# Kernel tuning notes

Measured on AMD Instinct MI355X. Metric: run time of the kernel, lower is better.

The kernel has to match this reference:

```python
import jax, jax.numpy as jnp
import numpy as np

B, S, H, E, V, EXTRA = 128, 512, 1024, 1024, 50000, 500
EPS = 1e-8


def setup_inputs() -> dict:
    key = jax.random.key(0)
    ks = jax.random.split(key, 32)
    sc = 0.02
    n = lambda k, sh: (jax.random.normal(k, sh, jnp.float32) * sc)
    return {
        'inputs': jax.random.randint(ks[0], (B, 1), 0, V),
        'dec_hidden': n(ks[1], (1, B, H)),
        'enc_outputs': n(ks[2], (B, S, H)),
        'enc_padding_mask': jnp.zeros((B, S), jnp.float32),
        'context_vector_t1': n(ks[3], (B, H)),
        'enc_batch_extend_vocab': jax.random.randint(ks[4], (B, S), 0, V + EXTRA),
        'extra_zeros': jnp.zeros((B, EXTRA), jnp.float32),
        'coverage': jax.random.uniform(ks[5], (B, S), jnp.float32) * 0.1,
        # parameters
        'embed': n(ks[6], (V, E)),
        'ln_g': jnp.ones((E,), jnp.float32),
        'ln_b': jnp.zeros((E,), jnp.float32),
        'xc_W': n(ks[7], (E, H + E)), 'xc_b': jnp.zeros((E,), jnp.float32),
        'W_ih': n(ks[8], (3 * H, E)), 'W_hh': n(ks[9], (3 * H, H)),
        'b_ih': jnp.zeros((3 * H,), jnp.float32), 'b_hh': jnp.zeros((3 * H,), jnp.float32),
        'Wh': n(ks[10], (H, H)),
        'Ws': n(ks[11], (H, H)), 'Ws_b': jnp.zeros((H,), jnp.float32),
        'Wc': n(ks[12], (H, 1)),
        'Vv': n(ks[13], (H,)),
        'pg_W': n(ks[14], (2 * H + E,)), 'pg_b': jnp.zeros((1,), jnp.float32),
        'out1_W': n(ks[15], (H, 2 * H)), 'out1_b': jnp.zeros((H,), jnp.float32),
        'out2_W': n(ks[16], (V, H)), 'out2_b': jnp.zeros((V,), jnp.float32),
    }


def _layernorm(x, g, b):
    mu = jnp.mean(x, axis=-1, keepdims=True)
    var = jnp.mean(jnp.square(x - mu), axis=-1, keepdims=True)
    return (x - mu) / jnp.sqrt(var + 1e-5) * g + b


def reference(inputs, dec_hidden, enc_outputs, enc_padding_mask, context_vector_t1,
              enc_batch_extend_vocab, extra_zeros, coverage,
              embed, ln_g, ln_b, xc_W, xc_b, W_ih, W_hh, b_ih, b_hh,
              Wh, Ws, Ws_b, Wc, Vv, pg_W, pg_b, out1_W, out1_b, out2_W, out2_b):
    # embedding + layernorm: [B, E]
    x = _layernorm(embed[inputs[:, 0]], ln_g, ln_b)
    # x_context: Linear(H+E -> E)
    x = jnp.concatenate([x, context_vector_t1], axis=1) @ xc_W.T + xc_b

    # single GRU step (torch gate order r, z, n)
    h0 = dec_hidden[0]  # [B, H]
    gx = x @ W_ih.T + b_ih
    gh = h0 @ W_hh.T + b_hh
    r = jax.nn.sigmoid(gx[:, :H] + gh[:, :H])
    z = jax.nn.sigmoid(gx[:, H:2 * H] + gh[:, H:2 * H])
    nn_ = jnp.tanh(gx[:, 2 * H:] + r * gh[:, 2 * H:])
    s_t = (1.0 - z) * nn_ + z * h0  # [B, H]; dec_output == s_t for 1-layer GRU
    dec_output = s_t

    # Bahdanau additive attention with coverage
    enc_feat = jnp.einsum('bsh,kh->bsk', enc_outputs, Wh)           # [B,S,H]
    dec_feat = s_t @ Ws.T + Ws_b                                     # [B,H]
    cov_feat = coverage[:, :, None] * Wc[:, 0][None, None, :]        # [B,S,H]
    e_t = jnp.einsum('bsh,h->bs', jnp.tanh(enc_feat + dec_feat[:, None, :] + cov_feat), Vv)
    atten_dist = jax.nn.softmax(e_t + enc_padding_mask, axis=1)      # [B,S]
    h_t = jnp.einsum('bs,bsh->bh', atten_dist, enc_outputs)          # [B,H]
    coverage_next = coverage + atten_dist

    # pointer generator gate
    p_gen_in = jnp.concatenate([h_t, s_t, x], axis=1)                # [B, 2H+E]
    p_gen = jnp.clip(jax.nn.sigmoid(p_gen_in @ pg_W + pg_b), EPS, None)[:, None]  # [B,1]

    # vocab distribution
    s_t_h_t = jnp.concatenate([dec_output, h_t], axis=1)             # [B,2H]
    logits = (s_t_h_t @ out1_W.T + out1_b) @ out2_W.T + out2_b       # [B,V]
    vocab_dist = jax.nn.softmax(logits, axis=1)

    # mix + scatter-add copy distribution over extended vocab
    vocab_dist_ = jnp.concatenate([p_gen * vocab_dist, extra_zeros], axis=1)  # [B, V+EXTRA]
    atten_dist_ = (1.0 - p_gen) * atten_dist
    rows = jnp.arange(B)[:, None]
    final_dist = vocab_dist_.at[rows, enc_batch_extend_vocab].add(atten_dist_)
    final_dist = jnp.clip(final_dist, EPS, None)

    coverage_loss = jnp.sum(jnp.minimum(atten_dist, coverage_next), axis=1)  # [B]
    return (jnp.log(final_dist), s_t[None], h_t, coverage_next, coverage_loss)
```

## Files before the change

### kernel.cpp

```cpp
#include <hip/hip_runtime.h>
#include <hip/hip_bf16.h>
#include <stdint.h>

#define B_ 128
#define S_ 512
#define H_ 1024
#define E_ 1024
#define V_ 50000
#define EXTRA_ 500
#define VE_ 50500
#define EPS_ 1e-8f

typedef __attribute__((ext_vector_type(4))) float f32x4;
typedef __attribute__((ext_vector_type(8))) short bf16x8;

__device__ __forceinline__ unsigned short f2bf(float f) {
    unsigned u = __builtin_bit_cast(unsigned, f);
    u = (u + 0x7FFFu + ((u >> 16) & 1u)) >> 16;
    return (unsigned short)u;
}

__device__ __forceinline__ bf16x8 pack8(const float* f) {
    union { bf16x8 v; unsigned short s[8]; } u;
#pragma unroll
    for (int i = 0; i < 8; ++i) u.s[i] = f2bf(f[i]);
    return u.v;
}

__device__ __forceinline__ float bf2f(unsigned short s) {
    unsigned u = (unsigned)s << 16;
    return __builtin_bit_cast(float, u);
}

__device__ __forceinline__ float fast_tanh(float x) {
    x = fminf(fmaxf(x, -15.f), 15.f);
    float e = __expf(2.f * x);
    return __fdividef(e - 1.f, e + 1.f);
}

__device__ __forceinline__ void gload16(const void* g, void* l) {
    __builtin_amdgcn_global_load_lds(
        reinterpret_cast<const __attribute__((address_space(1))) unsigned int*>(
            reinterpret_cast<uintptr_t>(g)),
        reinterpret_cast<__attribute__((address_space(3))) unsigned int*>(
            reinterpret_cast<uintptr_t>(l)),
        16, 0, 0);
}

__global__ __launch_bounds__(256) void cvt_bf16_kernel(const float* __restrict__ in,
                                                       unsigned short* __restrict__ out) {
    int i = (blockIdx.x * 256 + threadIdx.x) * 8;
    float f[8];
    *(float4*)f     = *(const float4*)(in + i);
    *(float4*)(f+4) = *(const float4*)(in + i + 4);
    union { uint4 v; unsigned short s[8]; } u;
#pragma unroll
    for (int j = 0; j < 8; ++j) u.s[j] = f2bf(f[j]);
    *(uint4*)(out + i) = u.v;
}

__global__ __launch_bounds__(256) void embed_ln_kernel(
    const int* __restrict__ tok, const float* __restrict__ embed,
    const float* __restrict__ g, const float* __restrict__ beta,
    const float* __restrict__ ctx, float* __restrict__ x_cat)
{
    __shared__ float red[256];
    int b = blockIdx.x, t = threadIdx.x;
    const float* row = embed + (size_t)tok[b] * E_;
    float v[4];
    float s = 0.f;
#pragma unroll
    for (int i = 0; i < 4; ++i) { v[i] = row[t + i*256]; s += v[i]; }
    red[t] = s; __syncthreads();
    for (int o = 128; o > 0; o >>= 1) { if (t < o) red[t] += red[t+o]; __syncthreads(); }
    float mu = red[0] * (1.f/E_);
    __syncthreads();
    s = 0.f;
#pragma unroll
    for (int i = 0; i < 4; ++i) { float d = v[i]-mu; s += d*d; }
    red[t] = s; __syncthreads();
    for (int o = 128; o > 0; o >>= 1) { if (t < o) red[t] += red[t+o]; __syncthreads(); }
    float inv = rsqrtf(red[0]*(1.f/E_) + 1e-5f);
    float* xrow = x_cat + (size_t)b * 2048;
#pragma unroll
    for (int i = 0; i < 4; ++i) {
        int j = t + i*256;
        xrow[j] = (v[i]-mu)*inv*g[j] + beta[j];
        xrow[1024 + j] = ctx[b*1024 + j];
    }
}

__global__ __launch_bounds__(256) void gemm128_kernel(
    const float* __restrict__ A, const float* __restrict__ W,
    const float* __restrict__ bias, float* __restrict__ C, float* __restrict__ C1,
    int N, int K, int ldc, int kchunk)
{
    __shared__ char Ab[128*64*2];
    __shared__ char Wb[64*64*2];
    const int t = threadIdx.x;
    const int wid = t >> 6, lane = t & 63;
    const int waveM = wid >> 1, waveN = wid & 1;
    const int lq = lane >> 4, lr = lane & 15;
    const int n0 = blockIdx.x * 64;
    const int kbeg = blockIdx.y * kchunk, kend = kbeg + kchunk;
    f32x4 acc[4][2];
#pragma unroll
    for (int i = 0; i < 4; ++i)
#pragma unroll
        for (int j = 0; j < 2; ++j) acc[i][j] = (f32x4){0.f,0.f,0.f,0.f};
    for (int kc = kbeg; kc < kend; kc += 64) {
        __syncthreads();
#pragma unroll
        for (int i = 0; i < 4; ++i) {
            int c = t + i*256;
            int row = c >> 3, k8 = (c & 7) << 3;
            const float* src = A + (size_t)row*K + kc + k8;
            float f[8];
            *(float4*)f     = *(const float4*)src;
            *(float4*)(f+4) = *(const float4*)(src+4);
            int byte = row*128 + ((k8*2) ^ ((row&7)<<4));
            *(bf16x8*)(Ab + byte) = pack8(f);
        }
#pragma unroll
        for (int i = 0; i < 2; ++i) {
            int c = t + i*256;
            int row = c >> 3, k8 = (c & 7) << 3;
            int n = n0 + row;
            float f[8] = {0,0,0,0,0,0,0,0};
            if (n < N) {
                const float* src = W + (size_t)n*K + kc + k8;
                *(float4*)f     = *(const float4*)src;
                *(float4*)(f+4) = *(const float4*)(src+4);
            }
            int byte = row*128 + ((k8*2) ^ ((row&7)<<4));
            *(bf16x8*)(Wb + byte) = pack8(f);
        }
        __syncthreads();
#pragma unroll
        for (int kf = 0; kf < 2; ++kf) {
            int kk2 = (kf*32 + (lq<<3)) * 2;
            bf16x8 bfr[2];
#pragma unroll
            for (int nf = 0; nf < 2; ++nf) {
                int r = waveN*32 + nf*16 + lr;
                bfr[nf] = *(const bf16x8*)(Wb + r*128 + (kk2 ^ ((r&7)<<4)));
            }
#pragma unroll
            for (int mf = 0; mf < 4; ++mf) {
                int r = waveM*64 + mf*16 + lr;
                bf16x8 afr = *(const bf16x8*)(Ab + r*128 + (kk2 ^ ((r&7)<<4)));
#pragma unroll
                for (int nf = 0; nf < 2; ++nf)
                    acc[mf][nf] = __builtin_amdgcn_mfma_f32_16x16x32_bf16(afr, bfr[nf], acc[mf][nf], 0, 0, 0);
            }
        }
    }
    float* Cp = (blockIdx.y == 0) ? C : (C1 + (size_t)(blockIdx.y - 1) * 128 * (size_t)ldc);
    bool addb = (bias != nullptr) && (blockIdx.y == 0);
#pragma unroll
    for (int mf = 0; mf < 4; ++mf)
#pragma unroll
        for (int nf = 0; nf < 2; ++nf) {
            int n = n0 + waveN*32 + nf*16 + lr;
            if (n < N) {
                float bv = addb ? bias[n] : 0.f;
#pragma unroll
                for (int r = 0; r < 4; ++r) {
                    int m = waveM*64 + mf*16 + (lq<<2) + r;
                    Cp[(size_t)m*ldc + n] = acc[mf][nf][r] + bv;
                }
            }
        }
}

__global__ __launch_bounds__(256) void reduce4_kernel(
    const float* __restrict__ in, float* __restrict__ out, int len)
{
    int i = blockIdx.x*256 + threadIdx.x;
    if (i < len) out[i] = in[i] + in[len+i] + in[2*len+i] + in[3*len+i];
}

__global__ __launch_bounds__(256) void gru_gate_kernel(
    const float* __restrict__ gxp, const float* __restrict__ ghp,
    const float* __restrict__ h0, float* __restrict__ s_t)
{
    int i = blockIdx.x*256 + threadIdx.x;
    int b = i >> 10, h = i & 1023;
    const float* gx0 = gxp + (size_t)b*3072;
    const float* gx1 = gx0 + 393216;
    const float* gh0 = ghp + (size_t)b*3072;
    const float* gh1 = gh0 + 393216;
    float grx = gx0[h] + gx1[h],        grh = gh0[h] + gh1[h];
    float gzx = gx0[h+1024]+gx1[h+1024], gzh = gh0[h+1024]+gh1[h+1024];
    float gnx = gx0[h+2048]+gx1[h+2048], gnh = gh0[h+2048]+gh1[h+2048];
    float r = 1.f/(1.f+__expf(-(grx + grh)));
    float z = 1.f/(1.f+__expf(-(gzx + gzh)));
    float n = fast_tanh(gnx + r*gnh);
    s_t[i] = (1.f-z)*n + z*h0[i];
}

__global__ __launch_bounds__(256,4) void attn_gemm_bf16_kernel(
    const unsigned short* __restrict__ encb,
    const unsigned short* __restrict__ whb,
    const float* __restrict__ dec_feat, const float* __restrict__ coverage,
    const float* __restrict__ Wc, const float* __restrict__ Vv,
    float* __restrict__ e_part)
{
    __shared__ char Ab[128*128];
    __shared__ char Bb[128*128];
    const int t = threadIdx.x;
    const int wid = t >> 6, lane = t & 63;
    const int waveM = wid >> 1, waveN = wid & 1;
    const int lq = lane >> 4, lr = lane & 15;
    int bid = blockIdx.x;
    int wg = (bid & 7) * 512 + (bid >> 3);
    const int nt = wg & 7, mt = wg >> 3;
    const int m0 = mt * 128, n0 = nt * 128;
    const int b = m0 >> 9;

    const int grow = wid*8 + (lane >> 3);
    const int gk16 = (lane & 7) ^ ((lane >> 3) & 7);
    const unsigned short* asrc = encb + (size_t)(m0 + grow)*H_ + gk16*8;
    const unsigned short* bsrc = whb  + (size_t)(n0 + grow)*H_ + gk16*8;
    char* aldst = Ab + wid*1024;
    char* bldst = Bb + wid*1024;

    f32x4 acc[4][4];
#pragma unroll
    for (int i = 0; i < 4; ++i)
#pragma unroll
        for (int j = 0; j < 4; ++j) acc[i][j] = (f32x4){0.f,0.f,0.f,0.f};

    for (int kc = 0; kc < 1024; kc += 64) {
        __syncthreads();
#pragma unroll
        for (int i = 0; i < 4; ++i) {
            gload16(asrc + kc + i*32*H_, aldst + i*4096);
            gload16(bsrc + kc + i*32*H_, bldst + i*4096);
        }
        __syncthreads();
#pragma unroll
        for (int kf = 0; kf < 2; ++kf) {
            const int koff = kf*64 + lq*16;
            bf16x8 bfr[4];
#pragma unroll
            for (int nf = 0; nf < 4; ++nf) {
                int r = waveN*64 + nf*16 + lr;
                bfr[nf] = *(const bf16x8*)(Bb + r*128 + (koff ^ ((r&7)<<4)));
            }
#pragma unroll
            for (int mf = 0; mf < 4; ++mf) {
                int r = waveM*64 + mf*16 + lr;
                bf16x8 afr = *(const bf16x8*)(Ab + r*128 + (koff ^ ((r&7)<<4)));
#pragma unroll
                for (int nf = 0; nf < 4; ++nf)
                    acc[mf][nf] = __builtin_amdgcn_mfma_f32_16x16x32_bf16(afr, bfr[nf], acc[mf][nf], 0, 0, 0);
            }
        }
    }
    float cv[4][4];
#pragma unroll
    for (int mf = 0; mf < 4; ++mf)
#pragma unroll
        for (int r = 0; r < 4; ++r) {
            int m = m0 + waveM*64 + mf*16 + lq*4 + r;
            cv[mf][r] = coverage[b*S_ + (m & 511)];
        }
    float e_acc[4][4] = {};
#pragma unroll
    for (int nf = 0; nf < 4; ++nf) {
        int n = n0 + waveN*64 + nf*16 + lr;
        float df = dec_feat[b*H_ + n];
        float wc = Wc[n];
        float vv = Vv[n];
#pragma unroll
        for (int mf = 0; mf < 4; ++mf)
#pragma unroll
            for (int r = 0; r < 4; ++r)
                e_acc[mf][r] += fast_tanh(acc[mf][nf][r] + df + cv[mf][r]*wc) * vv;
    }
#pragma unroll
    for (int msk = 1; msk < 16; msk <<= 1)
#pragma unroll
        for (int mf = 0; mf < 4; ++mf)
#pragma unroll
            for (int r = 0; r < 4; ++r)
                e_acc[mf][r] += __shfl_xor(e_acc[mf][r], msk);
    __syncthreads();
    float* el = (float*)Ab;
    if (lr == 0) {
#pragma unroll
        for (int mf = 0; mf < 4; ++mf)
#pragma unroll
            for (int r = 0; r < 4; ++r)
                el[waveN*128 + waveM*64 + mf*16 + lq*4 + r] = e_acc[mf][r];
    }
    __syncthreads();
    if (t < 128)
        e_part[(size_t)nt*65536 + m0 + t] = el[t] + el[128 + t];
}

__global__ __launch_bounds__(512,4) void attn_gemm_f32_kernel(
    const float* __restrict__ enc, const float* __restrict__ Wh,
    const float* __restrict__ dec_feat, const float* __restrict__ coverage,
    const float* __restrict__ Wc, const float* __restrict__ Vv,
    float* __restrict__ e_part)
{
    __shared__ char Ab[128*64*2];
    __shared__ char Bb[256*64*2];
    __shared__ float e_lds[4][128];
    const int t = threadIdx.x;
    const int wid = t >> 6, lane = t & 63;
    const int waveM = wid >> 2, waveN = wid & 3;
    const int lq = lane >> 4, lr = lane & 15;
    int bid = blockIdx.x;
    int wg = (bid & 7) * 256 + (bid >> 3);
    const int mt = wg >> 2, nt = wg & 3;
    const int m0 = mt * 128, n0 = nt * 256;
    const int b = m0 >> 9;
    const int arow = t >> 2, ak0 = (t & 3) * 16;
    const int brow = t >> 1, bk0 = (t & 1) * 32;
    f32x4 acc[4][4];
#pragma unroll
    for (int i = 0; i < 4; ++i)
#pragma unroll
        for (int j = 0; j < 4; ++j) acc[i][j] = (f32x4){0.f,0.f,0.f,0.f};
    for (int kc = 0; kc < 1024; kc += 64) {
        __syncthreads();
        {
            const float* src = enc + (size_t)(m0 + arow)*H_ + kc + ak0;
            float f[16];
            *(float4*)(f)    = *(const float4*)(src);
            *(float4*)(f+4)  = *(const float4*)(src+4);
            *(float4*)(f+8)  = *(const float4*)(src+8);
            *(float4*)(f+12) = *(const float4*)(src+12);
            char* dst = Ab + arow*128;
            int sw = (arow & 7) << 4;
            *(bf16x8*)(dst + ((ak0*2)      ^ sw)) = pack8(f);
            *(bf16x8*)(dst + ((ak0*2 + 16) ^ sw)) = pack8(f+8);
        }
        {
            const float* src = Wh + (size_t)(n0 + brow)*H_ + kc + bk0;
            char* dst = Bb + brow*128;
            int sw = (brow & 7) << 4;
            float f[16];
            *(float4*)(f)    = *(const float4*)(src);
            *(float4*)(f+4)  = *(const float4*)(src+4);
            *(float4*)(f+8)  = *(const float4*)(src+8);
            *(float4*)(f+12) = *(const float4*)(src+12);
            *(bf16x8*)(dst + ((bk0*2)      ^ sw)) = pack8(f);
            *(bf16x8*)(dst + ((bk0*2 + 16) ^ sw)) = pack8(f+8);
            *(float4*)(f)    = *(const float4*)(src+16);
            *(float4*)(f+4)  = *(const float4*)(src+20);
            *(float4*)(f+8)  = *(const float4*)(src+24);
            *(float4*)(f+12) = *(const float4*)(src+28);
            *(bf16x8*)(dst + ((bk0*2 + 32) ^ sw)) = pack8(f);
            *(bf16x8*)(dst + ((bk0*2 + 48) ^ sw)) = pack8(f+8);
        }
        __syncthreads();
#pragma unroll
        for (int kf = 0; kf < 2; ++kf) {
            const int koff = kf*64 + lq*16;
            bf16x8 bfr[4];
#pragma unroll
            for (int nf = 0; nf < 4; ++nf) {
                int r = waveN*64 + nf*16 + lr;
                bfr[nf] = *(const bf16x8*)(Bb + r*128 + (koff ^ ((r&7)<<4)));
            }
#pragma unroll
            for (int mf = 0; mf < 4; ++mf) {
                int r = waveM*64 + mf*16 + lr;
                bf16x8 afr = *(const bf16x8*)(Ab + r*128 + (koff ^ ((r&7)<<4)));
#pragma unroll
                for (int nf = 0; nf < 4; ++nf)
                    acc[mf][nf] = __builtin_amdgcn_mfma_f32_16x16x32_bf16(afr, bfr[nf], acc[mf][nf], 0, 0, 0);
            }
        }
    }
    float cv[4][4];
#pragma unroll
    for (int mf = 0; mf < 4; ++mf)
#pragma unroll
        for (int r = 0; r < 4; ++r) {
            int m = m0 + waveM*64 + mf*16 + lq*4 + r;
            cv[mf][r] = coverage[b*S_ + (m & 511)];
        }
    float e_acc[4][4] = {};
#pragma unroll
    for (int nf = 0; nf < 4; ++nf) {
        int n = n0 + waveN*64 + nf*16 + lr;
        float df = dec_feat[b*H_ + n];
        float wc = Wc[n];
        float vv = Vv[n];
#pragma unroll
        for (int mf = 0; mf < 4; ++mf)
#pragma unroll
            for (int r = 0; r < 4; ++r)
                e_acc[mf][r] += fast_tanh(acc[mf][nf][r] + df + cv[mf][r]*wc) * vv;
    }
#pragma unroll
    for (int msk = 1; msk < 16; msk <<= 1)
#pragma unroll
        for (int mf = 0; mf < 4; ++mf)
#pragma unroll
            for (int r = 0; r < 4; ++r)
                e_acc[mf][r] += __shfl_xor(e_acc[mf][r], msk);
    if (lr == 0) {
#pragma unroll
        for (int mf = 0; mf < 4; ++mf)
#pragma unroll
            for (int r = 0; r < 4; ++r)
                e_lds[waveN][waveM*64 + mf*16 + lq*4 + r] = e_acc[mf][r];
    }
    __syncthreads();
    if (t < 128)
        e_part[(size_t)nt*65536 + m0 + t] = e_lds[0][t] + e_lds[1][t] + e_lds[2][t] + e_lds[3][t];
}

__global__ __launch_bounds__(256) void attn_softmax_kernel(
    const float* __restrict__ e_part, int np, const float* __restrict__ mask,
    const float* __restrict__ cov, float* __restrict__ att,
    float* __restrict__ cov_next, float* __restrict__ loss)
{
    __shared__ float red[256];
    int b = blockIdx.x, t = threadIdx.x;
    int i1 = b*S_ + t, i2 = i1 + 256;
    float e1 = mask[i1], e2 = mask[i2];
    for (int p = 0; p < np; ++p) { e1 += e_part[(size_t)p*65536 + i1]; e2 += e_part[(size_t)p*65536 + i2]; }
    red[t] = fmaxf(e1, e2); __syncthreads();
    for (int o = 128; o > 0; o >>= 1) { if (t < o) red[t] = fmaxf(red[t], red[t+o]); __syncthreads(); }
    float m = red[0]; __syncthreads();
    float a1 = __expf(e1-m), a2 = __expf(e2-m);
    red[t] = a1+a2; __syncthreads();
    for (int o = 128; o > 0; o >>= 1) { if (t < o) red[t] += red[t+o]; __syncthreads(); }
    float inv = 1.f/red[0]; __syncthreads();
    a1 *= inv; a2 *= inv;
    att[i1] = a1; att[i2] = a2;
    float c1 = cov[i1]+a1, c2 = cov[i2]+a2;
    cov_next[i1] = c1; cov_next[i2] = c2;
    red[t] = fminf(a1,c1)+fminf(a2,c2); __syncthreads();
    for (int o = 128; o > 0; o >>= 1) { if (t < o) red[t] += red[t+o]; __syncthreads(); }
    if (t == 0) loss[b] = red[0];
}

__global__ __launch_bounds__(256) void context_part_bf16_kernel(
    const float* __restrict__ att, const unsigned short* __restrict__ encb, float* __restrict__ hq)
{
    __shared__ float asl[128];
    int b = blockIdx.x, sub = blockIdx.y;
    int hh = sub & 1, q = sub >> 1;
    int t = threadIdx.x;
    if (t < 128) asl[t] = att[b*S_ + q*128 + t];
    __syncthreads();
    int h = hh*512 + t*2;
    const unsigned short* ep = encb + (size_t)b*S_*H_ + (size_t)q*128*H_ + h;
    float a0 = 0.f, a1 = 0.f;
#pragma unroll 4
    for (int s = 0; s < 128; ++s) {
        union { unsigned u; unsigned short s2[2]; } v;
        v.u = *(const unsigned*)(ep + (size_t)s*H_);
        float w = asl[s];
        a0 += w*bf2f(v.s2[0]); a1 += w*bf2f(v.s2[1]);
    }
    float* o = hq + ((size_t)q*B_ + b)*H_ + h;
    o[0] = a0; o[1] = a1;
}

__global__ __launch_bounds__(256) void context_part_f32_kernel(
    const float* __restrict__ att, const float* __restrict__ enc, float* __restrict__ hq)
{
    __shared__ float asl[128];
    int b = blockIdx.x, sub = blockIdx.y;
    int hh = sub & 1, q = sub >> 1;
    int t = threadIdx.x;
    if (t < 128) asl[t] = att[b*S_ + q*128 + t];
    __syncthreads();
    int h = hh*512 + t*2;
    const float* ep = enc + (size_t)b*S_*H_ + (size_t)q*128*H_ + h;
    float a0 = 0.f, a1 = 0.f;
#pragma unroll 4
    for (int s = 0; s < 128; ++s) {
        float2 v = *(const float2*)(ep + (size_t)s*H_);
        float w = asl[s];
        a0 += w*v.x; a1 += w*v.y;
    }
    float* o = hq + ((size_t)q*B_ + b)*H_ + h;
    o[0] = a0; o[1] = a1;
}

__global__ __launch_bounds__(256) void pgen_kernel(
    const float* __restrict__ h_t, const float* __restrict__ s_t, const float* __restrict__ x,
    const float* __restrict__ pgW, const float* __restrict__ pgb,
    float* __restrict__ pgen, float* __restrict__ A2)
{
    __shared__ float red[256];
    int b = blockIdx.x, t = threadIdx.x;
    float s = 0.f;
#pragma unroll
    for (int i = 0; i < 12; ++i) {
        int j = t + i*256;
        float v = (j < 1024) ? h_t[b*1024+j] : (j < 2048 ? s_t[b*1024 + j-1024] : x[b*1024 + j-2048]);
        s += v * pgW[j];
    }
    red[t] = s; __syncthreads();
    for (int o = 128; o > 0; o >>= 1) { if (t < o) red[t] += red[t+o]; __syncthreads(); }
    if (t == 0) {
        float p = 1.f/(1.f+__expf(-(red[0] + pgb[0])));
        pgen[b] = fmaxf(p, EPS_);
    }
#pragma unroll
    for (int i = 0; i < 8; ++i) {
        int j = t + i*256;
        A2[(size_t)b*2048 + j] = (j < 1024) ? s_t[b*1024+j] : h_t[b*1024+j-1024];
    }
}

__global__ __launch_bounds__(256) void vocab_pass1_kernel(
    const float* __restrict__ logits, float2* __restrict__ mpart)
{
    __shared__ float rm[256], rl[256];
    int b = blockIdx.x, c = blockIdx.y, t = threadIdx.x;
    int lo = c * 12625;
    int hi = min(lo + 12625, V_);
    const float* row = logits + (size_t)b*VE_;
    float m = -1e30f, l = 0.f;
    for (int i = lo + t; i < hi; i += 256) {
        float v = row[i];
        if (v > m) { l = l*__expf(m-v) + 1.f; m = v; }
        else l += __expf(v-m);
    }
    rm[t] = m; rl[t] = l; __syncthreads();
    for (int o = 128; o > 0; o >>= 1) {
        if (t < o) {
            float m1 = rm[t], m2 = rm[t+o];
            float M = fmaxf(m1, m2);
            rl[t] = rl[t]*__expf(m1-M) + rl[t+o]*__expf(m2-M);
            rm[t] = M;
        }
        __syncthreads();
    }
    if (t == 0) mpart[b*4 + c] = make_float2(rm[0], rl[0]);
}

__global__ __launch_bounds__(256) void vocab_pass2_kernel(
    const float* __restrict__ logits, const float2* __restrict__ mpart,
    const float* __restrict__ pgen, const int* __restrict__ ebev,
    const float* __restrict__ att, float* __restrict__ out0)
{
    __shared__ unsigned bmap[395];
    __shared__ unsigned hkey[1024];
    __shared__ float hval[1024];
    int b = blockIdx.x, c = blockIdx.y, t = threadIdx.x;
    int lo = c * 12625, hi = lo + 12625;
    float2 p0 = mpart[b*4+0], p1 = mpart[b*4+1], p2 = mpart[b*4+2], p3 = mpart[b*4+3];
    float M = fmaxf(fmaxf(p0.x, p1.x), fmaxf(p2.x, p3.x));
    float L = p0.y*__expf(p0.x-M) + p1.y*__expf(p1.x-M) + p2.y*__expf(p2.x-M) + p3.y*__expf(p3.x-M);
    float pg = pgen[b];
    float inv = pg / L;
    for (int i = t; i < 395; i += 256) bmap[i] = 0u;
    for (int i = t; i < 1024; i += 256) { hkey[i] = 0xFFFFFFFFu; hval[i] = 0.f; }
    __syncthreads();
    for (int s = t; s < 512; s += 256) {
        int col = ebev[b*S_ + s];
        if (col >= lo && col < hi) {
            float v = (1.f - pg) * att[b*S_ + s];
            unsigned cl = (unsigned)(col - lo);
            atomicOr(&bmap[cl >> 5], 1u << (cl & 31));
            unsigned slot = (cl * 2654435761u >> 16) & 1023u;
            while (true) {
                unsigned old = atomicCAS(&hkey[slot], 0xFFFFFFFFu, cl);
                if (old == 0xFFFFFFFFu || old == cl) { atomicAdd(&hval[slot], v); break; }
                slot = (slot + 1) & 1023u;
            }
        }
    }
    __syncthreads();
    const float* row = logits + (size_t)b*VE_;
    float* orow = out0 + (size_t)b*VE_;
    for (int i = lo + t; i < hi; i += 256) {
        float base = 0.f;
        if (i < V_) base = __expf(row[i] - M) * inv;
        unsigned cl = (unsigned)(i - lo);
        if (bmap[cl >> 5] & (1u << (cl & 31))) {
            unsigned slot = (cl * 2654435761u >> 16) & 1023u;
            while (hkey[slot] != cl) slot = (slot + 1) & 1023u;
            base += hval[slot];
        }
        orow[i] = __logf(fmaxf(base, EPS_));
    }
}

extern "C" void kernel_launch(void* const* d_in, const int* in_sizes, int n_in,
                              void* d_out, int out_size, void* d_ws, size_t ws_size,
                              hipStream_t stream) {
    const int*   tok        = (const int*)d_in[0];
    const float* dec_hidden = (const float*)d_in[1];
    const float* enc        = (const float*)d_in[2];
    const float* mask       = (const float*)d_in[3];
    const float* ctx1       = (const float*)d_in[4];
    const int*   ebev       = (const int*)d_in[5];
    const float* cov        = (const float*)d_in[7];
    const float* embed      = (const float*)d_in[8];
    const float* ln_g       = (const float*)d_in[9];
    const float* ln_b       = (const float*)d_in[10];
    const float* xc_W       = (const float*)d_in[11];
    const float* xc_b       = (const float*)d_in[12];
    const float* W_ih       = (const float*)d_in[13];
    const float* W_hh       = (const float*)d_in[14];
    const float* b_ih       = (const float*)d_in[15];
    const float* b_hh       = (const float*)d_in[16];
    const float* Wh         = (const float*)d_in[17];
    const float* Ws         = (const float*)d_in[18];
    const float* Ws_b       = (const float*)d_in[19];
    const float* Wc         = (const float*)d_in[20];
    const float* Vv         = (const float*)d_in[21];
    const float* pg_W       = (const float*)d_in[22];
    const float* pg_b       = (const float*)d_in[23];
    const float* out1_W     = (const float*)d_in[24];
    const float* out1_b     = (const float*)d_in[25];
    const float* out2_W     = (const float*)d_in[26];
    const float* out2_b     = (const float*)d_in[27];

    float* out      = (float*)d_out;
    float* s_t      = out + 6464000;
    float* h_t      = out + 6595072;
    float* cov_next = out + 6726144;
    float* loss     = out + 6791680;

    const size_t ENC_SLOTS = 33554432, WH_SLOTS = 524288;
    const size_t BASE_SLOTS = 5178496;
    const size_t need = (ENC_SLOTS + WH_SLOTS + BASE_SLOTS) * 4;
    const bool bf16_path = (ws_size >= need);

    float* wsf = (float*)d_ws;
    unsigned short* enc_bf = (unsigned short*)d_ws;
    unsigned short* wh_bf  = (unsigned short*)(wsf + ENC_SLOTS);
    float* base     = bf16_path ? (wsf + ENC_SLOTS + WH_SLOTS) : wsf;
    float* x_cat    = base;
    float* x_part   = base + 262144;
    float* x        = base + 786432;
    float* gx_part  = base + 917504;
    float* gh_part  = base + 1703936;
    float* ds_part  = base + 2490368;
    float* dec_feat = base + 3014656;
    float* e_part   = base + 3145728;
    float* att      = base + 3670016;
    float* pgen     = base + 3735552;
    float* A2       = base + 3735680;
    float* h2_part  = base + 3997824;
    float* h2       = base + 4522112;
    float* hq       = base + 4653184;
    float2* mpart   = (float2*)(base + 5177472);

    if (bf16_path) {
        cvt_bf16_kernel<<<32768, 256, 0, stream>>>(enc, enc_bf);
        cvt_bf16_kernel<<<512, 256, 0, stream>>>(Wh, wh_bf);
    }
    embed_ln_kernel<<<128, 256, 0, stream>>>(tok, embed, ln_g, ln_b, ctx1, x_cat);
    gemm128_kernel<<<dim3(16,4), 256, 0, stream>>>(x_cat, xc_W, xc_b, x_part, x_part + 131072, 1024, 2048, 1024, 512);
    reduce4_kernel<<<512, 256, 0, stream>>>(x_part, x, 131072);
    gemm128_kernel<<<dim3(48,2), 256, 0, stream>>>(x, W_ih, b_ih, gx_part, gx_part + 393216, 3072, 1024, 3072, 512);
    gemm128_kernel<<<dim3(48,2), 256, 0, stream>>>(dec_hidden, W_hh, b_hh, gh_part, gh_part + 393216, 3072, 1024, 3072, 512);
    gru_gate_kernel<<<512, 256, 0, stream>>>(gx_part, gh_part, dec_hidden, s_t);
    gemm128_kernel<<<dim3(16,4), 256, 0, stream>>>(s_t, Ws, Ws_b, ds_part, ds_part + 131072, 1024, 1024, 1024, 256);
    reduce4_kernel<<<512, 256, 0, stream>>>(ds_part, dec_feat, 131072);

    int npart;
    if (bf16_path) {
        attn_gemm_bf16_kernel<<<4096, 256, 0, stream>>>(enc_bf, wh_bf, dec_feat, cov, Wc, Vv, e_part);
        npart = 8;
    } else {
        attn_gemm_f32_kernel<<<2048, 512, 0, stream>>>(enc, Wh, dec_feat, cov, Wc, Vv, e_part);
        npart = 4;
    }
    attn_softmax_kernel<<<128, 256, 0, stream>>>(e_part, npart, mask, cov, att, cov_next, loss);
    dim3 g8(128, 8);
    if (bf16_path)
        context_part_bf16_kernel<<<g8, 256, 0, stream>>>(att, enc_bf, hq);
    else
        context_part_f32_kernel<<<g8, 256, 0, stream>>>(att, enc, hq);
    reduce4_kernel<<<512, 256, 0, stream>>>(hq, h_t, 131072);
    pgen_kernel<<<128, 256, 0, stream>>>(h_t, s_t, x, pg_W, pg_b, pgen, A2);
    gemm128_kernel<<<dim3(16,4), 256, 0, stream>>>(A2, out1_W, out1_b, h2_part, h2_part + 131072, 1024, 2048, 1024, 512);
    reduce4_kernel<<<512, 256, 0, stream>>>(h2_part, h2, 131072);

    gemm128_kernel<<<dim3(782,1), 256, 0, stream>>>(h2, out2_W, out2_b, out, nullptr, 50000, 1024, VE_, 1024);
    vocab_pass1_kernel<<<dim3(128,4), 256, 0, stream>>>(out, mpart);
    vocab_pass2_kernel<<<dim3(128,4), 256, 0, stream>>>(out, mpart, pgen, ebev, att, out);
}
```

Measured before the change: 532.1 us.

## Fuse split-K partial reductions into consumers and widen bf16 context loads

The split-K reduction for dec_feat is folded into the attention GEMM epilogue, and the h_t reduction is folded into pgen_kernel, which also builds A2 in the same pass. This removes two reduce4 launches and their intermediate buffers. The bf16 context kernel now loads 16-byte vectors with 4 blocks per batch row, combining two half-sequence partials in LDS. The attention GEMM launch bound rises to 5 waves per SIMD, which may force register spills.

```diff
diff --git a/kernel.cpp b/kernel.cpp
--- a/kernel.cpp
+++ b/kernel.cpp
@@ -92,7 +92,7 @@
 
 __global__ __launch_bounds__(256) void gemm128_kernel(
     const float* __restrict__ A, const float* __restrict__ W,
-    const float* __restrict__ bias, float* __restrict__ C, float* __restrict__ C1,
+    const float* __restrict__ bias, float* __restrict__ C,
     int N, int K, int ldc, int kchunk)
 {
     __shared__ char Ab[128*64*2];
@@ -155,7 +155,7 @@
             }
         }
     }
-    float* Cp = (blockIdx.y == 0) ? C : (C1 + (size_t)(blockIdx.y - 1) * 128 * (size_t)ldc);
+    float* Cp = C + (size_t)blockIdx.y * 128 * (size_t)ldc;
     bool addb = (bias != nullptr) && (blockIdx.y == 0);
 #pragma unroll
     for (int mf = 0; mf < 4; ++mf)
@@ -199,10 +199,11 @@
     s_t[i] = (1.f-z)*n + z*h0[i];
 }
 
-__global__ __launch_bounds__(256,4) void attn_gemm_bf16_kernel(
+__global__ __launch_bounds__(256,5) void attn_gemm_bf16_kernel(
     const unsigned short* __restrict__ encb,
     const unsigned short* __restrict__ whb,
-    const float* __restrict__ dec_feat, const float* __restrict__ coverage,
+    const float* __restrict__ ds_part,
+    const float* __restrict__ coverage,
     const float* __restrict__ Wc, const float* __restrict__ Vv,
     float* __restrict__ e_part)
 {
@@ -270,7 +271,8 @@
 #pragma unroll
     for (int nf = 0; nf < 4; ++nf) {
         int n = n0 + waveN*64 + nf*16 + lr;
-        float df = dec_feat[b*H_ + n];
+        const float* dsp = ds_part + b*H_ + n;
+        float df = dsp[0] + dsp[131072] + dsp[262144] + dsp[393216];
         float wc = Wc[n];
         float vv = Vv[n];
 #pragma unroll
@@ -302,7 +304,7 @@
 
 __global__ __launch_bounds__(512,4) void attn_gemm_f32_kernel(
     const float* __restrict__ enc, const float* __restrict__ Wh,
-    const float* __restrict__ dec_feat, const float* __restrict__ coverage,
+    const float* __restrict__ ds_part, const float* __restrict__ coverage,
     const float* __restrict__ Wc, const float* __restrict__ Vv,
     float* __restrict__ e_part)
 {
@@ -389,7 +391,8 @@
 #pragma unroll
     for (int nf = 0; nf < 4; ++nf) {
         int n = n0 + waveN*64 + nf*16 + lr;
-        float df = dec_feat[b*H_ + n];
+        const float* dsp = ds_part + b*H_ + n;
+        float df = dsp[0] + dsp[131072] + dsp[262144] + dsp[393216];
         float wc = Wc[n];
         float vv = Vv[n];
 #pragma unroll
@@ -447,23 +450,35 @@
     const float* __restrict__ att, const unsigned short* __restrict__ encb, float* __restrict__ hq)
 {
     __shared__ float asl[128];
-    int b = blockIdx.x, sub = blockIdx.y;
-    int hh = sub & 1, q = sub >> 1;
-    int t = threadIdx.x;
+    __shared__ float cpart[128][9];
+    int b = blockIdx.x, q = blockIdx.y, t = threadIdx.x;
     if (t < 128) asl[t] = att[b*S_ + q*128 + t];
     __syncthreads();
-    int h = hh*512 + t*2;
-    const unsigned short* ep = encb + (size_t)b*S_*H_ + (size_t)q*128*H_ + h;
-    float a0 = 0.f, a1 = 0.f;
-#pragma unroll 4
-    for (int s = 0; s < 128; ++s) {
-        union { unsigned u; unsigned short s2[2]; } v;
-        v.u = *(const unsigned*)(ep + (size_t)s*H_);
-        float w = asl[s];
-        a0 += w*bf2f(v.s2[0]); a1 += w*bf2f(v.s2[1]);
-    }
-    float* o = hq + ((size_t)q*B_ + b)*H_ + h;
-    o[0] = a0; o[1] = a1;
+    int lane = t & 127, su = t >> 7;
+    int hc = lane * 8;
+    const unsigned short* ep = encb + ((size_t)(b*S_ + q*128 + su*64))*H_ + hc;
+    float acc[8] = {};
+#pragma unroll 2
+    for (int s = 0; s < 64; ++s) {
+        uint4 v = *(const uint4*)(ep + (size_t)s*H_);
+        float w = asl[su*64 + s];
+        const unsigned short* pv = (const unsigned short*)&v;
+#pragma unroll
+        for (int k = 0; k < 8; ++k) acc[k] += w * bf2f(pv[k]);
+    }
+    if (su == 1) {
+#pragma unroll
+        for (int k = 0; k < 8; ++k) cpart[lane][k] = acc[k];
+    }
+    __syncthreads();
+    if (su == 0) {
+        float o[8];
+#pragma unroll
+        for (int k = 0; k < 8; ++k) o[k] = acc[k] + cpart[lane][k];
+        float* dst = hq + (size_t)q*131072 + (size_t)b*1024 + hc;
+        *(float4*)dst     = *(float4*)o;
+        *(float4*)(dst+4) = *(float4*)(o+4);
+    }
 }
 
 __global__ __launch_bounds__(256) void context_part_f32_kernel(
@@ -489,29 +504,29 @@
 }
 
 __global__ __launch_bounds__(256) void pgen_kernel(
-    const float* __restrict__ h_t, const float* __restrict__ s_t, const float* __restrict__ x,
+    const float* __restrict__ hq, const float* __restrict__ s_t, const float* __restrict__ x,
     const float* __restrict__ pgW, const float* __restrict__ pgb,
-    float* __restrict__ pgen, float* __restrict__ A2)
+    float* __restrict__ pgen, float* __restrict__ h_t, float* __restrict__ A2)
 {
     __shared__ float red[256];
     int b = blockIdx.x, t = threadIdx.x;
-    float s = 0.f;
-#pragma unroll
-    for (int i = 0; i < 12; ++i) {
+    float dot = 0.f;
+#pragma unroll
+    for (int i = 0; i < 4; ++i) {
         int j = t + i*256;
-        float v = (j < 1024) ? h_t[b*1024+j] : (j < 2048 ? s_t[b*1024 + j-1024] : x[b*1024 + j-2048]);
-        s += v * pgW[j];
-    }
-    red[t] = s; __syncthreads();
+        const float* hp = hq + (size_t)b*1024 + j;
+        float hv = hp[0] + hp[131072] + hp[262144] + hp[393216];
+        float sv = s_t[b*1024 + j];
+        h_t[b*1024 + j] = hv;
+        A2[(size_t)b*2048 + j] = sv;
+        A2[(size_t)b*2048 + 1024 + j] = hv;
+        dot += hv*pgW[j] + sv*pgW[1024+j] + x[b*1024+j]*pgW[2048+j];
+    }
+    red[t] = dot; __syncthreads();
     for (int o = 128; o > 0; o >>= 1) { if (t < o) red[t] += red[t+o]; __syncthreads(); }
     if (t == 0) {
         float p = 1.f/(1.f+__expf(-(red[0] + pgb[0])));
         pgen[b] = fmaxf(p, EPS_);
-    }
-#pragma unroll
-    for (int i = 0; i < 8; ++i) {
-        int j = t + i*256;
-        A2[(size_t)b*2048 + j] = (j < 1024) ? s_t[b*1024+j] : h_t[b*1024+j-1024];
     }
 }
 
@@ -642,7 +657,6 @@
     float* gx_part  = base + 917504;
     float* gh_part  = base + 1703936;
     float* ds_part  = base + 2490368;
-    float* dec_feat = base + 3014656;
     float* e_part   = base + 3145728;
     float* att      = base + 3670016;
     float* pgen     = base + 3735552;
@@ -657,34 +671,34 @@
         cvt_bf16_kernel<<<512, 256, 0, stream>>>(Wh, wh_bf);
     }
     embed_ln_kernel<<<128, 256, 0, stream>>>(tok, embed, ln_g, ln_b, ctx1, x_cat);
-    gemm128_kernel<<<dim3(16,4), 256, 0, stream>>>(x_cat, xc_W, xc_b, x_part, x_part + 131072, 1024, 2048, 1024, 512);
+    gemm128_kernel<<<dim3(16,4), 256, 0, stream>>>(x_cat, xc_W, xc_b, x_part, 1024, 2048, 1024, 512);
     reduce4_kernel<<<512, 256, 0, stream>>>(x_part, x, 131072);
-    gemm128_kernel<<<dim3(48,2), 256, 0, stream>>>(x, W_ih, b_ih, gx_part, gx_part + 393216, 3072, 1024, 3072, 512);
-    gemm128_kernel<<<dim3(48,2), 256, 0, stream>>>(dec_hidden, W_hh, b_hh, gh_part, gh_part + 393216, 3072, 1024, 3072, 512);
+    gemm128_kernel<<<dim3(48,2), 256, 0, stream>>>(x, W_ih, b_ih, gx_part, 3072, 1024, 3072, 512);
+    gemm128_kernel<<<dim3(48,2), 256, 0, stream>>>(dec_hidden, W_hh, b_hh, gh_part, 3072, 1024, 3072, 512);
     gru_gate_kernel<<<512, 256, 0, stream>>>(gx_part, gh_part, dec_hidden, s_t);
-    gemm128_kernel<<<dim3(16,4), 256, 0, stream>>>(s_t, Ws, Ws_b, ds_part, ds_part + 131072, 1024, 1024, 1024, 256);
-    reduce4_kernel<<<512, 256, 0, stream>>>(ds_part, dec_feat, 131072);
+    gemm128_kernel<<<dim3(16,4), 256, 0, stream>>>(s_t, Ws, Ws_b, ds_part, 1024, 1024, 1024, 256);
 
     int npart;
     if (bf16_path) {
-        attn_gemm_bf16_kernel<<<4096, 256, 0, stream>>>(enc_bf, wh_bf, dec_feat, cov, Wc, Vv, e_part);
+        attn_gemm_bf16_kernel<<<4096, 256, 0, stream>>>(enc_bf, wh_bf, ds_part, cov, Wc, Vv, e_part);
         npart = 8;
     } else {
-        attn_gemm_f32_kernel<<<2048, 512, 0, stream>>>(enc, Wh, dec_feat, cov, Wc, Vv, e_part);
+        attn_gemm_f32_kernel<<<2048, 512, 0, stream>>>(enc, Wh, ds_part, cov, Wc, Vv, e_part);
         npart = 4;
     }
     attn_softmax_kernel<<<128, 256, 0, stream>>>(e_part, npart, mask, cov, att, cov_next, loss);
-    dim3 g8(128, 8);
-    if (bf16_path)
+    if (bf16_path) {
+        dim3 g8(128, 4);
         context_part_bf16_kernel<<<g8, 256, 0, stream>>>(att, enc_bf, hq);
-    else
+    } else {
+        dim3 g8(128, 8);
         context_part_f32_kernel<<<g8, 256, 0, stream>>>(att, enc, hq);
-    reduce4_kernel<<<512, 256, 0, stream>>>(hq, h_t, 131072);
-    pgen_kernel<<<128, 256, 0, stream>>>(h_t, s_t, x, pg_W, pg_b, pgen, A2);
-    gemm128_kernel<<<dim3(16,4), 256, 0, stream>>>(A2, out1_W, out1_b, h2_part, h2_part + 131072, 1024, 2048, 1024, 512);
+    }
+    pgen_kernel<<<128, 256, 0, stream>>>(hq, s_t, x, pg_W, pg_b, pgen, h_t, A2);
+    gemm128_kernel<<<dim3(16,4), 256, 0, stream>>>(A2, out1_W, out1_b, h2_part, 1024, 2048, 1024, 512);
     reduce4_kernel<<<512, 256, 0, stream>>>(h2_part, h2, 131072);
 
-    gemm128_kernel<<<dim3(782,1), 256, 0, stream>>>(h2, out2_W, out2_b, out, nullptr, 50000, 1024, VE_, 1024);
+    gemm128_kernel<<<dim3(782,1), 256, 0, stream>>>(h2, out2_W, out2_b, out, 50000, 1024, VE_, 1024);
     vocab_pass1_kernel<<<dim3(128,4), 256, 0, stream>>>(out, mpart);
     vocab_pass2_kernel<<<dim3(128,4), 256, 0, stream>>>(out, mpart, pgen, ebev, att, out);
 }
```

New measurement: 977.4 us. +83.7%, slower.
